# Kernel tuning notes

Hardware: AMD Instinct MI355X
Metric: run time of the kernel (lower is better)

## Reference

```python
import jax, jax.numpy as jnp
import numpy as np

EMBED = 1024
HEADS = 16
INTERNAL = 1024  # embedding_dim // downsample_rate
HEAD_DIM = INTERNAL // HEADS


def setup_inputs() -> dict:
    key = jax.random.key(0)
    ks = jax.random.split(key, 12)
    B, S = 2, 2048
    s_in = 1.0 / np.sqrt(EMBED)
    s_out = 1.0 / np.sqrt(INTERNAL)
    return {
        "queries": jax.random.normal(ks[0], (B, S, EMBED), jnp.float32),
        "keys": jax.random.normal(ks[1], (B, S, EMBED), jnp.float32),
        "values": jax.random.normal(ks[2], (B, S, EMBED), jnp.float32),
        "Wq": jax.random.uniform(ks[3], (EMBED, INTERNAL), jnp.float32, -s_in, s_in),
        "bq": jax.random.uniform(ks[4], (INTERNAL,), jnp.float32, -s_in, s_in),
        "Wk": jax.random.uniform(ks[5], (EMBED, INTERNAL), jnp.float32, -s_in, s_in),
        "bk": jax.random.uniform(ks[6], (INTERNAL,), jnp.float32, -s_in, s_in),
        "Wv": jax.random.uniform(ks[7], (EMBED, INTERNAL), jnp.float32, -s_in, s_in),
        "bv": jax.random.uniform(ks[8], (INTERNAL,), jnp.float32, -s_in, s_in),
        "Wo": jax.random.uniform(ks[9], (INTERNAL, EMBED), jnp.float32, -s_out, s_out),
        "bo": jax.random.uniform(ks[10], (EMBED,), jnp.float32, -s_out, s_out),
    }


def _split_heads(x):
    B, S, D = x.shape
    return x.reshape(B, S, HEADS, D // HEADS).transpose(0, 2, 1, 3)  # bhsd


def reference(queries, keys, values, Wq, bq, Wk, bk, Wv, bv, Wo, bo):
    q = _split_heads(queries @ Wq + bq)
    k = _split_heads(keys @ Wk + bk)
    v = _split_heads(values @ Wv + bv)
    # NOTE: original scales by 1/sqrt(internal_dim), not 1/sqrt(head_dim)
    scale = 1.0 / np.sqrt(INTERNAL).astype(np.float32)
    scores = jnp.einsum("bhqd,bhkd->bhqk", q, k) * scale
    probs = jax.nn.softmax(scores, axis=-1)
    out = jnp.einsum("bhqk,bhkd->bhqd", probs, v)
    B, H, S, Dh = out.shape
    out = out.transpose(0, 2, 1, 3).reshape(B, S, H * Dh)
    return out @ Wo + bo
```

## Files before the change

kernel.cpp:

```cpp
#include <hip/hip_runtime.h>
#include <stdint.h>

typedef unsigned short u16;
typedef __attribute__((ext_vector_type(8))) short short8;
typedef __attribute__((ext_vector_type(4))) float f32x4;
typedef __attribute__((ext_vector_type(16))) float f32x16;
typedef __attribute__((ext_vector_type(8))) unsigned short u16x8;
typedef __attribute__((ext_vector_type(4))) unsigned short u16x4;
typedef __attribute__((ext_vector_type(4))) uint32_t u32x4;

#if __has_builtin(__builtin_amdgcn_exp2f)
#define EXP2(x) __builtin_amdgcn_exp2f(x)
#else
#define EXP2(x) exp2f(x)
#endif

__device__ __forceinline__ u16 f2bf(float f) {
  union { float f; uint32_t u; } v; v.f = f;
  uint32_t r = (v.u + 0x7FFFu + ((v.u >> 16) & 1u)) >> 16;
  return (u16)r;
}

__device__ __forceinline__ uint32_t pack2(float a, float b) {
  return (__float_as_uint(b) & 0xffff0000u) | (__float_as_uint(a) >> 16);
}

__device__ __forceinline__ void gload_lds16(const void* g, void* l) {
  __builtin_amdgcn_global_load_lds(
      (const __attribute__((address_space(1))) void*)g,
      (__attribute__((address_space(3))) void*)l,
      16, 0, 0);
}

__global__ __launch_bounds__(256) void cvt_x(const float* __restrict__ q,
                                             const float* __restrict__ k,
                                             const float* __restrict__ v,
                                             u16* __restrict__ dst) {
  const float* src = blockIdx.z == 0 ? q : (blockIdx.z == 1 ? k : v);
  u16* d = dst + (size_t)blockIdx.z * (4096u * 1024u);
  size_t i = ((size_t)blockIdx.x * 256 + threadIdx.x) * 8;
  float4 a = *(const float4*)(src + i);
  float4 b = *(const float4*)(src + i + 4);
  u16x8 o;
  o[0] = f2bf(a.x); o[1] = f2bf(a.y); o[2] = f2bf(a.z); o[3] = f2bf(a.w);
  o[4] = f2bf(b.x); o[5] = f2bf(b.y); o[6] = f2bf(b.z); o[7] = f2bf(b.w);
  *(u16x8*)(d + i) = o;
}

__global__ __launch_bounds__(256) void cvt_wt(const float* __restrict__ Wq,
                                              const float* __restrict__ Wk,
                                              const float* __restrict__ Wv,
                                              const float* __restrict__ Wo,
                                              u16* __restrict__ Wt4) {
  const float* W = blockIdx.z == 0 ? Wq : (blockIdx.z == 1 ? Wk
                   : (blockIdx.z == 2 ? Wv : Wo));
  u16* Wt = Wt4 + (size_t)blockIdx.z * (1024u * 1024u);
  __shared__ u16 tile[64][65];
  int kt = blockIdx.x * 64, nt = blockIdx.y * 64;
  int t = threadIdx.x;
#pragma unroll
  for (int r = 0; r < 4; ++r) {
    int id = t + r * 256;
    int kk = id >> 4, c4 = id & 15;
    float4 vv = *(const float4*)(W + (size_t)(kt + kk) * 1024 + nt + c4 * 4);
    tile[kk][c4 * 4 + 0] = f2bf(vv.x);
    tile[kk][c4 * 4 + 1] = f2bf(vv.y);
    tile[kk][c4 * 4 + 2] = f2bf(vv.z);
    tile[kk][c4 * 4 + 3] = f2bf(vv.w);
  }
  __syncthreads();
#pragma unroll
  for (int r = 0; r < 4; ++r) {
    int id = t + r * 256;
    int n = id >> 4, kc = id & 15;
    u16x4 o;
    o[0] = tile[kc * 4 + 0][n];
    o[1] = tile[kc * 4 + 1][n];
    o[2] = tile[kc * 4 + 2][n];
    o[3] = tile[kc * 4 + 3][n];
    *(u16x4*)(Wt + (size_t)(nt + n) * 1024 + kt + kc * 4) = o;
  }
}

template <bool F32OUT>
__device__ __forceinline__ void gemm_tile(const u16* __restrict__ A,
                                          const u16* __restrict__ Bt,
                                          const float* __restrict__ bias,
                                          u16* __restrict__ Cb,
                                          float* __restrict__ Cf,
                                          float scale, int bm, int bn) {
  __shared__ u16 Alds[128 * 64];
  __shared__ u16 Blds[128 * 64];
  const int tid = threadIdx.x;
  const int lane = tid & 63, w = tid >> 6;
  const int wm = (w >> 1) * 64, wn = (w & 1) * 64;
  const int l15 = lane & 15, lg = lane >> 4;

  f32x4 acc[4][4] = {};

  int srow[4], scol[4], soff[4];
#pragma unroll
  for (int i = 0; i < 4; ++i) {
    int o = (w * 4 + i) * 1024 + lane * 16;
    int row = o >> 7;
    int kc = ((o >> 4) & 7) ^ (row & 7);
    srow[i] = row; scol[i] = kc * 8; soff[i] = o;
  }

  for (int kt = 0; kt < 16; ++kt) {
    __syncthreads();
#pragma unroll
    for (int i = 0; i < 4; ++i) {
      gload_lds16(A + (size_t)(bm * 128 + srow[i]) * 1024 + kt * 64 + scol[i],
                  (char*)Alds + soff[i]);
      gload_lds16(Bt + (size_t)(bn * 128 + srow[i]) * 1024 + kt * 64 + scol[i],
                  (char*)Blds + soff[i]);
    }
    __syncthreads();
#pragma unroll
    for (int ks = 0; ks < 2; ++ks) {
      short8 af[4], bf[4];
#pragma unroll
      for (int m = 0; m < 4; ++m) {
        int r = wm + m * 16 + l15;
        int byt = r * 128 + ((ks * 64 + lg * 16) ^ ((r & 7) << 4));
        af[m] = *(const short8*)((const char*)Alds + byt);
      }
#pragma unroll
      for (int n = 0; n < 4; ++n) {
        int r = wn + n * 16 + l15;
        int byt = r * 128 + ((ks * 64 + lg * 16) ^ ((r & 7) << 4));
        bf[n] = *(const short8*)((const char*)Blds + byt);
      }
#pragma unroll
      for (int m = 0; m < 4; ++m)
#pragma unroll
        for (int n = 0; n < 4; ++n)
          acc[m][n] = __builtin_amdgcn_mfma_f32_16x16x32_bf16(
              af[m], bf[n], acc[m][n], 0, 0, 0);
    }
  }
#pragma unroll
  for (int m = 0; m < 4; ++m) {
    int row0 = bm * 128 + wm + m * 16 + lg * 4;
#pragma unroll
    for (int n = 0; n < 4; ++n) {
      int col = bn * 128 + wn + n * 16 + l15;
      float bvv = bias[col];
#pragma unroll
      for (int r = 0; r < 4; ++r) {
        float v = (acc[m][n][r] + bvv) * scale;
        if (F32OUT)
          Cf[(size_t)(row0 + r) * 1024 + col] = v;
        else
          Cb[(size_t)(row0 + r) * 1024 + col] = f2bf(v);
      }
    }
  }
}

__global__ __launch_bounds__(256) void proj_kernel(const u16* __restrict__ X3,
                                                   const u16* __restrict__ Wt3,
                                                   const float* __restrict__ bq,
                                                   const float* __restrict__ bk,
                                                   const float* __restrict__ bv,
                                                   u16* __restrict__ out3) {
  int z = blockIdx.z;
  const float* bias = z == 0 ? bq : (z == 1 ? bk : bv);
  float scale = z == 0 ? 0.045084220f : 1.0f;
  gemm_tile<false>(X3 + (size_t)z * 4096 * 1024, Wt3 + (size_t)z * 1024 * 1024,
                   bias, out3 + (size_t)z * 4096 * 1024, nullptr, scale,
                   blockIdx.x, blockIdx.y);
}

__global__ __launch_bounds__(256) void outproj_kernel(const u16* __restrict__ Att,
                                                      const u16* __restrict__ Wot,
                                                      const float* __restrict__ bo,
                                                      float* __restrict__ out) {
  gemm_tile<true>(Att, Wot, bo, nullptr, out, 1.0f, blockIdx.x, blockIdx.y);
}

__global__ __launch_bounds__(256) void vt_kernel(const u16* __restrict__ v,
                                                 u16* __restrict__ vt) {
  int bh = blockIdx.y;
  int sbase = blockIdx.x * 64;
  int b = bh >> 4, h = bh & 15;
  __shared__ u16 tile[64][65];
  int t = threadIdx.x;
#pragma unroll
  for (int r = 0; r < 2; ++r) {
    int id = t + r * 256;
    int s = id >> 3, dc = id & 7;
    u16x8 x = *(const u16x8*)(v + (size_t)(b * 2048 + sbase + s) * 1024 +
                              h * 64 + dc * 8);
#pragma unroll
    for (int j = 0; j < 8; ++j) tile[s][dc * 8 + j] = x[j];
  }
  __syncthreads();
#pragma unroll
  for (int r = 0; r < 2; ++r) {
    int id = t + r * 256;
    int d = id >> 3, sc = id & 7;
    u16x8 o;
#pragma unroll
    for (int j = 0; j < 8; ++j) o[j] = tile[sc * 8 + j][d];
    *(u16x8*)(vt + ((size_t)bh * 64 + d) * 2048 + sbase + sc * 8) = o;
  }
}

__global__ __launch_bounds__(128) void attn_kernel(const u16* __restrict__ q,
                                                   const u16* __restrict__ k,
                                                   const u16* __restrict__ vt,
                                                   u16* __restrict__ att) {
  __shared__ u16 smem[8192];
  const int tid = threadIdx.x, lane = tid & 63, w = tid >> 6;
  const int l31 = lane & 31, hi = lane >> 5;
  const int bh = blockIdx.y, b = bh >> 4, h = bh & 15;
  const int qb = blockIdx.x * 64 + w * 32;

  short8 qf[4];
  const u16* qrow = q + (size_t)(b * 2048 + qb + l31) * 1024 + h * 64 + hi * 8;
#pragma unroll
  for (int s = 0; s < 4; ++s) qf[s] = *(const short8*)(qrow + s * 16);

  f32x16 acc0 = {}, acc1 = {};
  float lsum = 0.f;

  int srow[4], scol[4], soff[4];
#pragma unroll
  for (int i = 0; i < 4; ++i) {
    int o = w * 4096 + i * 1024 + lane * 16;
    int row = o >> 7;
    int kc = ((o >> 4) & 7) ^ (row & 7);
    srow[i] = row; scol[i] = kc * 8; soff[i] = o;
  }
  const u16* ksrc = k + (size_t)b * 2048 * 1024 + h * 64;
  const u16* vsrc = vt + (size_t)bh * 64 * 2048;
  const char* KL = (const char*)smem;
  const char* VL = (const char*)smem + 8192;

  for (int t = 0; t < 32; ++t) {
    const int kbase = t * 64;
    __syncthreads();
#pragma unroll
    for (int i = 0; i < 4; ++i) {
      gload_lds16(ksrc + (size_t)(kbase + srow[i]) * 1024 + scol[i],
                  (char*)smem + soff[i]);
      gload_lds16(vsrc + (size_t)srow[i] * 2048 + kbase + scol[i],
                  (char*)smem + 8192 + soff[i]);
    }
    __syncthreads();

#pragma unroll
    for (int kg = 0; kg < 2; ++kg) {
      f32x16 sc = {};
#pragma unroll
      for (int s = 0; s < 4; ++s) {
        int row = kg * 32 + l31;
        int byt = row * 128 + ((s * 32 + hi * 16) ^ ((row & 7) << 4));
        short8 ak = *(const short8*)(KL + byt);
        sc = __builtin_amdgcn_mfma_f32_32x32x16_bf16(ak, qf[s], sc, 0, 0, 0);
      }
      uint32_t pw_[4][2];
#pragma unroll
      for (int g = 0; g < 4; ++g) {
        float p0 = EXP2(sc[4 * g + 0]);
        float p1 = EXP2(sc[4 * g + 1]);
        float p2 = EXP2(sc[4 * g + 2]);
        float p3 = EXP2(sc[4 * g + 3]);
        lsum += (p0 + p1) + (p2 + p3);
        pw_[g][0] = pack2(p0, p1);
        pw_[g][1] = pack2(p2, p3);
      }
#pragma unroll
      for (int c = 0; c < 2; ++c) {
        uint32_t s0 = hi ? pw_[2 * c][0] : pw_[2 * c + 1][0];
        uint32_t s1 = hi ? pw_[2 * c][1] : pw_[2 * c + 1][1];
        uint32_t r0 = (uint32_t)__shfl_xor((int)s0, 32);
        uint32_t r1 = (uint32_t)__shfl_xor((int)s1, 32);
        u32x4 fw;
        fw[0] = hi ? r0 : pw_[2 * c][0];
        fw[1] = hi ? r1 : pw_[2 * c][1];
        fw[2] = hi ? pw_[2 * c + 1][0] : r0;
        fw[3] = hi ? pw_[2 * c + 1][1] : r1;
        short8 pf = __builtin_bit_cast(short8, fw);
        int colv = kg * 64 + c * 32 + hi * 16;
        {
          int row = l31;
          int byt = row * 128 + (colv ^ ((row & 7) << 4));
          short8 bv_ = *(const short8*)(VL + byt);
          acc0 = __builtin_amdgcn_mfma_f32_32x32x16_bf16(pf, bv_, acc0, 0, 0, 0);
        }
        {
          int row = 32 + l31;
          int byt = row * 128 + (colv ^ ((row & 7) << 4));
          short8 bv_ = *(const short8*)(VL + byt);
          acc1 = __builtin_amdgcn_mfma_f32_32x32x16_bf16(pf, bv_, acc1, 0, 0, 0);
        }
      }
    }
  }

  float ltot = lsum + __shfl_xor(lsum, 32);
  float rinv = 1.0f / ltot;
  __syncthreads();
  u16* tw = smem + w * 2048;
#pragma unroll
  for (int r = 0; r < 16; ++r) {
    int row = (r & 3) + 8 * (r >> 2) + 4 * hi;
    float ri = __shfl(rinv, row);
    tw[row * 64 + l31] = (u16)(__float_as_uint(acc0[r] * ri) >> 16);
    tw[row * 64 + 32 + l31] = (u16)(__float_as_uint(acc1[r] * ri) >> 16);
  }
  asm volatile("s_waitcnt lgkmcnt(0)" ::: "memory");
  u16* abase = att + (size_t)(b * 2048 + qb) * 1024 + h * 64;
#pragma unroll
  for (int i = 0; i < 4; ++i) {
    int id = lane + i * 64;
    int row = id >> 3, ch = id & 7;
    u16x8 vv = *(const u16x8*)(tw + row * 64 + ch * 8);
    *(u16x8*)(abase + (size_t)row * 1024 + ch * 8) = vv;
  }
}

extern "C" void kernel_launch(void* const* d_in, const int* in_sizes, int n_in,
                              void* d_out, int out_size, void* d_ws,
                              size_t ws_size, hipStream_t stream) {
  const float* Q  = (const float*)d_in[0];
  const float* K  = (const float*)d_in[1];
  const float* V  = (const float*)d_in[2];
  const float* Wq = (const float*)d_in[3];
  const float* bq = (const float*)d_in[4];
  const float* Wk = (const float*)d_in[5];
  const float* bk = (const float*)d_in[6];
  const float* Wv = (const float*)d_in[7];
  const float* bv = (const float*)d_in[8];
  const float* Wo = (const float*)d_in[9];
  const float* bo = (const float*)d_in[10];
  float* out = (float*)d_out;

  u16* ws = (u16*)d_ws;
  const size_t SZX = (size_t)4096 * 1024;
  const size_t SZW = (size_t)1024 * 1024;
  u16* Xbf   = ws;
  u16* Wtbf  = ws + 3 * SZX;
  u16* QKVbf = Wtbf + 4 * SZW;
  u16* VTbf  = QKVbf + 3 * SZX;
  u16* ATTbf = VTbf + SZX;

  hipLaunchKernelGGL(cvt_x, dim3(2048, 1, 3), dim3(256), 0, stream, Q, K, V,
                     Xbf);
  hipLaunchKernelGGL(cvt_wt, dim3(16, 16, 4), dim3(256), 0, stream, Wq, Wk, Wv,
                     Wo, Wtbf);
  hipLaunchKernelGGL(proj_kernel, dim3(32, 8, 3), dim3(256), 0, stream, Xbf,
                     Wtbf, bq, bk, bv, QKVbf);
  hipLaunchKernelGGL(vt_kernel, dim3(32, 32), dim3(256), 0, stream,
                     QKVbf + 2 * SZX, VTbf);
  hipLaunchKernelGGL(attn_kernel, dim3(32, 32), dim3(128), 0, stream, QKVbf,
                     QKVbf + SZX, VTbf, ATTbf);
  hipLaunchKernelGGL(outproj_kernel, dim3(32, 8), dim3(256), 0, stream, ATTbf,
                     Wtbf + 3 * SZW, bo, out);
}
```

Baseline: 147.2 us.

## Double attention block to four waves and drop cross-half shuffles via K row permutation

Each attention block now runs four waves over 128 queries, so every K/V tile staged in LDS is shared by twice as many query rows and cooperative loads take two iterations per thread instead of four. K rows are loaded in a permuted order so the score MFMA output layout lines up directly with the PV MFMA operand layout. This removes the per-step lane-xor shuffles and selects used to rearrange probabilities. Grid size halves to 512 blocks, which reduces parallelism, and correctness depends on the row permutation matching the MFMA layout exactly.

```diff
diff --git a/kernel.cpp b/kernel.cpp
--- a/kernel.cpp
+++ b/kernel.cpp
@@ -208,7 +208,7 @@
   }
 }
 
-__global__ __launch_bounds__(128) void attn_kernel(const u16* __restrict__ q,
+__global__ __launch_bounds__(256) void attn_kernel(const u16* __restrict__ q,
                                                    const u16* __restrict__ k,
                                                    const u16* __restrict__ vt,
                                                    u16* __restrict__ att) {
@@ -216,7 +216,7 @@
   const int tid = threadIdx.x, lane = tid & 63, w = tid >> 6;
   const int l31 = lane & 31, hi = lane >> 5;
   const int bh = blockIdx.y, b = bh >> 4, h = bh & 15;
-  const int qb = blockIdx.x * 64 + w * 32;
+  const int qb = blockIdx.x * 128 + w * 32;
 
   short8 qf[4];
   const u16* qrow = q + (size_t)(b * 2048 + qb + l31) * 1024 + h * 64 + hi * 8;
@@ -226,13 +226,14 @@
   f32x16 acc0 = {}, acc1 = {};
   float lsum = 0.f;
 
-  int srow[4], scol[4], soff[4];
-#pragma unroll
-  for (int i = 0; i < 4; ++i) {
-    int o = w * 4096 + i * 1024 + lane * 16;
+  int soff[2], krow[2], vrow[2], scol[2];
+#pragma unroll
+  for (int i = 0; i < 2; ++i) {
+    int o = i * 4096 + tid * 16;
     int row = o >> 7;
     int kc = ((o >> 4) & 7) ^ (row & 7);
-    srow[i] = row; scol[i] = kc * 8; soff[i] = o;
+    soff[i] = o; scol[i] = kc * 8; vrow[i] = row;
+    krow[i] = row ^ (((((row >> 2) ^ (row >> 3)) & 1)) ? 12 : 0);
   }
   const u16* ksrc = k + (size_t)b * 2048 * 1024 + h * 64;
   const u16* vsrc = vt + (size_t)bh * 64 * 2048;
@@ -243,10 +244,10 @@
     const int kbase = t * 64;
     __syncthreads();
 #pragma unroll
-    for (int i = 0; i < 4; ++i) {
-      gload_lds16(ksrc + (size_t)(kbase + srow[i]) * 1024 + scol[i],
+    for (int i = 0; i < 2; ++i) {
+      gload_lds16(ksrc + (size_t)(kbase + krow[i]) * 1024 + scol[i],
                   (char*)smem + soff[i]);
-      gload_lds16(vsrc + (size_t)srow[i] * 2048 + kbase + scol[i],
+      gload_lds16(vsrc + (size_t)vrow[i] * 2048 + kbase + scol[i],
                   (char*)smem + 8192 + soff[i]);
     }
     __syncthreads();
@@ -261,39 +262,29 @@
         short8 ak = *(const short8*)(KL + byt);
         sc = __builtin_amdgcn_mfma_f32_32x32x16_bf16(ak, qf[s], sc, 0, 0, 0);
       }
-      uint32_t pw_[4][2];
-#pragma unroll
-      for (int g = 0; g < 4; ++g) {
-        float p0 = EXP2(sc[4 * g + 0]);
-        float p1 = EXP2(sc[4 * g + 1]);
-        float p2 = EXP2(sc[4 * g + 2]);
-        float p3 = EXP2(sc[4 * g + 3]);
-        lsum += (p0 + p1) + (p2 + p3);
-        pw_[g][0] = pack2(p0, p1);
-        pw_[g][1] = pack2(p2, p3);
-      }
+      float p[16];
+#pragma unroll
+      for (int g = 0; g < 16; ++g) p[g] = EXP2(sc[g]);
+#pragma unroll
+      for (int g = 0; g < 16; g += 4)
+        lsum += (p[g] + p[g + 1]) + (p[g + 2] + p[g + 3]);
 #pragma unroll
       for (int c = 0; c < 2; ++c) {
-        uint32_t s0 = hi ? pw_[2 * c][0] : pw_[2 * c + 1][0];
-        uint32_t s1 = hi ? pw_[2 * c][1] : pw_[2 * c + 1][1];
-        uint32_t r0 = (uint32_t)__shfl_xor((int)s0, 32);
-        uint32_t r1 = (uint32_t)__shfl_xor((int)s1, 32);
         u32x4 fw;
-        fw[0] = hi ? r0 : pw_[2 * c][0];
-        fw[1] = hi ? r1 : pw_[2 * c][1];
-        fw[2] = hi ? pw_[2 * c + 1][0] : r0;
-        fw[3] = hi ? pw_[2 * c + 1][1] : r1;
+        fw[0] = pack2(p[8 * c + 0], p[8 * c + 1]);
+        fw[1] = pack2(p[8 * c + 2], p[8 * c + 3]);
+        fw[2] = pack2(p[8 * c + 4], p[8 * c + 5]);
+        fw[3] = pack2(p[8 * c + 6], p[8 * c + 7]);
         short8 pf = __builtin_bit_cast(short8, fw);
         int colv = kg * 64 + c * 32 + hi * 16;
         {
-          int row = l31;
-          int byt = row * 128 + (colv ^ ((row & 7) << 4));
+          int byt = l31 * 128 + (colv ^ ((l31 & 7) << 4));
           short8 bv_ = *(const short8*)(VL + byt);
           acc0 = __builtin_amdgcn_mfma_f32_32x32x16_bf16(pf, bv_, acc0, 0, 0, 0);
         }
         {
-          int row = 32 + l31;
-          int byt = row * 128 + (colv ^ ((row & 7) << 4));
+          int r1 = 32 + l31;
+          int byt = r1 * 128 + (colv ^ ((r1 & 7) << 4));
           short8 bv_ = *(const short8*)(VL + byt);
           acc1 = __builtin_amdgcn_mfma_f32_32x32x16_bf16(pf, bv_, acc1, 0, 0, 0);
         }
@@ -313,6 +304,7 @@
     tw[row * 64 + 32 + l31] = (u16)(__float_as_uint(acc1[r] * ri) >> 16);
   }
   asm volatile("s_waitcnt lgkmcnt(0)" ::: "memory");
+  __builtin_amdgcn_sched_barrier(0);
   u16* abase = att + (size_t)(b * 2048 + qb) * 1024 + h * 64;
 #pragma unroll
   for (int i = 0; i < 4; ++i) {
@@ -356,7 +348,7 @@
                      Wtbf, bq, bk, bv, QKVbf);
   hipLaunchKernelGGL(vt_kernel, dim3(32, 32), dim3(256), 0, stream,
                      QKVbf + 2 * SZX, VTbf);
-  hipLaunchKernelGGL(attn_kernel, dim3(32, 32), dim3(128), 0, stream, QKVbf,
+  hipLaunchKernelGGL(attn_kernel, dim3(16, 32), dim3(256), 0, stream, QKVbf,
                      QKVbf + SZX, VTbf, ATTbf);
   hipLaunchKernelGGL(outproj_kernel, dim3(32, 8), dim3(256), 0, stream, ATTbf,
                      Wtbf + 3 * SZW, bo, out);
```

After: 132.2 us. -10.2%, faster.
